# Kernel optimization log

Measured on AMD Instinct MI355X. Metric: run time of the kernel, lower is better.

The kernel has to match this reference:

```python
import jax, jax.numpy as jnp
import numpy as np

N_PTS = 20000  # points per cloud


def setup_inputs() -> dict:
    key = jax.random.key(0)
    k1, k2 = jax.random.split(key)
    preds = jax.random.normal(k1, (N_PTS, 3), dtype=jnp.float32)
    gts = jax.random.normal(k2, (1, N_PTS, 3), dtype=jnp.float32)
    return {"preds": preds, "gts": gts}


def reference(preds, gts):
    # x = gts: [B, Nx, 3]; y = preds.unsqueeze(0): [1, Ny, 3] (B must be 1 for bmm)
    y = preds[None]                                   # [1, Ny, 3]
    x = gts                                           # [1, Nx, 3]
    xx = jnp.sum(x * x, axis=-1)                      # [1, Nx]  (diag of x x^T)
    yy = jnp.sum(y * y, axis=-1)                      # [1, Ny]
    zz = jnp.einsum('bnd,bmd->bnm', x, y)             # [1, Nx, Ny]
    P = xx[:, :, None] + yy[:, None, :] - 2.0 * zz    # [1, Nx, Ny] squared dists
    dist1 = jnp.min(P, axis=1)                        # [1, Ny] min over gts points
    dist2 = jnp.min(P, axis=2)                        # [1, Nx] min over pred points
    idx1 = jnp.argmin(P, axis=1)                      # [1, Ny]
    idx2 = jnp.argmin(P, axis=2)                      # [1, Nx]
    return dist1, dist2, idx1, idx2
```

## Files before the change

kernel.cpp:

```cpp
#include <hip/hip_runtime.h>

#define N_PTS  20000
#define NG     128
#define NC     (NG * NG)
#define GMIN   (-6.0f)
#define GINV   (NG / 12.0f)
#define MARGIN 5e-4f
#define SSTRIDE (N_PTS / 64)
#define QB79   79

__device__ __forceinline__ float np_self_dot(float x, float y, float z) {
    return __fadd_rn(__fadd_rn(__fmul_rn(x, x), __fmul_rn(y, y)),
                     __fmul_rn(z, z));
}
__device__ __forceinline__ unsigned ordmap(float f) {
    unsigned b = __float_as_uint(f);
    return (b & 0x80000000u) ? ~b : (b | 0x80000000u);
}
__device__ __forceinline__ float invord(unsigned h) {
    return __uint_as_float((h & 0x80000000u) ? (h ^ 0x80000000u) : ~h);
}
__device__ __forceinline__ int cellC(float v) {
    int c = (int)((v - GMIN) * GINV);
    return c < 0 ? 0 : (c > NG - 1 ? NG - 1 : c);
}
__device__ __forceinline__ unsigned long long wave_min_u64(unsigned long long k) {
    #pragma unroll
    for (int m = 1; m < 64; m <<= 1) {
        unsigned long long o = __shfl_xor(k, m, 64);
        k = (o < k) ? o : k;
    }
    return k;
}

#define EVALQ(r, QX, QY, QZ, SQ, KEY)                                      \
    {   float sr = np_self_dot((r).x, (r).y, (r).z);                       \
        float zz = __fadd_rn(__fadd_rn(__fmul_rn(QX, (r).x),               \
                                       __fmul_rn(QY, (r).y)),              \
                             __fmul_rn(QZ, (r).z));                        \
        float P  = __fsub_rn(__fadd_rn(SQ, sr), __fadd_rn(zz, zz));        \
        unsigned long long kk =                                            \
            ((unsigned long long)ordmap(P) << 32) | __float_as_uint((r).w);\
        KEY = (kk < KEY) ? kk : KEY; }

#define SCAN_ROWS32(BND, ROWS, QX, QY, QZ, SQ, KEY)                        \
    for (int r0 = 0; r0 < (ROWS); r0 += 3) {                               \
        int i1 = r0 + 1 < (ROWS) ? r0 + 1 : (ROWS) - 1;                    \
        int i2 = r0 + 2 < (ROWS) ? r0 + 2 : (ROWS) - 1;                    \
        int L0 = __shfl(BND, r0, 64), H0 = __shfl(BND, 32 + r0, 64);       \
        int L1 = __shfl(BND, i1, 64), H1 = __shfl(BND, 32 + i1, 64);       \
        int L2 = __shfl(BND, i2, 64), H2 = __shfl(BND, 32 + i2, 64);       \
        int d0 = H0 - L0;                                                  \
        int d1 = (r0 + 1 < (ROWS)) ? H1 - L1 : 0;                          \
        int d2 = (r0 + 2 < (ROWS)) ? H2 - L2 : 0;                          \
        int s01 = d0 + d1, tot = s01 + d2;                                 \
        int t = lane;                                                      \
        if (t < tot) {                                                     \
            int p = t < d0 ? L0 + t : t < s01 ? L1 + (t - d0)              \
                                              : L2 + (t - s01);            \
            float4 rc = rs[p];                                             \
            for (t += 64; t < tot; t += 64) {                              \
                int pn = t < d0 ? L0 + t : t < s01 ? L1 + (t - d0)         \
                                                   : L2 + (t - s01);       \
                float4 rn = rs[pn];                                        \
                EVALQ(rc, QX, QY, QZ, SQ, KEY)                             \
                rc = rn;                                                   \
            }                                                              \
            EVALQ(rc, QX, QY, QZ, SQ, KEY)                                 \
        }                                                                  \
    }

#define SCAN_RECT(xL, xR, yL, yR, QX, QY, QZ, SQ, KEY)                     \
    {   int R = (xR) - (xL) + 1;                                           \
        for (int g = 0; g < R; g += 32) {                                  \
            int rows = R - g; if (rows > 32) rows = 32;                    \
            int xr  = (xL) + g + (l31 < rows ? l31 : rows - 1);            \
            int col = (lane < 32) ? (yL) : ((yR) + 1);                     \
            int b2 = cs[xr * NG + col];                                    \
            SCAN_ROWS32(b2, rows, QX, QY, QZ, SQ, KEY)                     \
        }                                                                  \
    }

__global__ __launch_bounds__(256) void k_hist(
    const float* __restrict__ preds, const float* __restrict__ gts,
    int* __restrict__ cursor)
{
    int t = blockIdx.x * 256 + threadIdx.x;
    if (t >= 2 * N_PTS) return;
    int cl = t / N_PTS, i = t - cl * N_PTS;
    const float* src = cl ? gts : preds;
    int cell = cellC(src[i*3+0]) * NG + cellC(src[i*3+1]);
    atomicAdd(&cursor[cl * NC + cell], 1);
}

__global__ __launch_bounds__(1024) void k_scan(
    int* __restrict__ cursor, int* __restrict__ bstart)
{
    __shared__ int wsum[16];
    __shared__ int wpre[16];
    int cl = blockIdx.x, t = threadIdx.x;
    int wave = t >> 6, lane = t & 63;

    int base = cl * NC + t * 16;
    const int4* c4 = (const int4*)(cursor + base);
    int4 a = c4[0], b = c4[1], c = c4[2], d = c4[3];
    int v[16] = { a.x, a.y, a.z, a.w, b.x, b.y, b.z, b.w,
                  c.x, c.y, c.z, c.w, d.x, d.y, d.z, d.w };
    int s = 0;
    #pragma unroll
    for (int i = 0; i < 16; ++i) s += v[i];

    int ps = s;
    #pragma unroll
    for (int m = 1; m < 64; m <<= 1) {
        int o = __shfl_up(ps, m, 64);
        if (lane >= m) ps += o;
    }
    if (lane == 63) wsum[wave] = ps;
    __syncthreads();
    if (t < 16) {
        int x = wsum[t];
        int px = x;
        #pragma unroll
        for (int m = 1; m < 16; m <<= 1) {
            int o = __shfl_up(px, m, 16);
            if ((t & 15) >= m) px += o;
        }
        wpre[t] = px - x;
    }
    __syncthreads();

    int run = wpre[wave] + (ps - s);
    #pragma unroll
    for (int i = 0; i < 16; ++i) {
        bstart[cl * (NC + 1) + t * 16 + i] = run;
        cursor[base + i] = run;
        run += v[i];
    }
    if (t == 1023) bstart[cl * (NC + 1) + NC] = run;
}

__global__ __launch_bounds__(256) void k_scatter(
    const float* __restrict__ preds, const float* __restrict__ gts,
    int* __restrict__ cursor, float4* __restrict__ sorted)
{
    int t = blockIdx.x * 256 + threadIdx.x;
    if (t >= 2 * N_PTS) return;
    int cl = t / N_PTS, i = t - cl * N_PTS;
    const float* src = cl ? gts : preds;
    float x = src[i*3+0], y = src[i*3+1], z = src[i*3+2];
    int cell = cellC(x) * NG + cellC(y);
    int pos = atomicAdd(&cursor[cl * NC + cell], 1);
    sorted[(size_t)cl * N_PTS + pos] = make_float4(x, y, z, __int_as_float(i));
}

__global__ __launch_bounds__(64) void k_main(
    const float4* __restrict__ sorted, const int* __restrict__ bstart,
    float* __restrict__ out)
{
    int wid  = blockIdx.x;
    int lane = threadIdx.x;
    int q0   = wid * 2;
    int dir  = q0 / N_PTS;
    int qp0  = q0 - dir * N_PTS;
    int rcl  = 1 - dir;

    const float4* rs = sorted + (size_t)rcl * N_PTS;
    const int*    cs = bstart + rcl * (NC + 1);

    float4 samp = rs[lane * SSTRIDE];
    float4 qva  = sorted[(size_t)dir * N_PTS + qp0];
    float4 qvb  = sorted[(size_t)dir * N_PTS + qp0 + 1];
    int oa = __float_as_int(qva.w), ob = __float_as_int(qvb.w);
    float qax = qva.x, qay = qva.y, qaz = qva.z;
    float qbx = qvb.x, qby = qvb.y, qbz = qvb.z;
    float sqa = np_self_dot(qax, qay, qaz);
    float sqb = np_self_dot(qbx, qby, qbz);

    unsigned long long ka = ~0ULL, kb = ~0ULL;
    int l31 = lane & 31;

    int cxa = cellC(qax), cya = cellC(qay);
    int cxb = cellC(qbx), cyb = cellC(qby);
    int sxLa = cxa > 1 ? cxa - 2 : 0, sxRa = cxa < NG-2 ? cxa + 2 : NG-1;
    int syLa = cya > 1 ? cya - 2 : 0, syRa = cya < NG-2 ? cya + 2 : NG-1;
    int sxLb = cxb > 1 ? cxb - 2 : 0, sxRb = cxb < NG-2 ? cxb + 2 : NG-1;
    int syLb = cyb > 1 ? cyb - 2 : 0, syRb = cyb < NG-2 ? cyb + 2 : NG-1;
    int nrsA = sxRa - sxLa + 1, nrsB = sxRb - sxLb + 1;
    int xrA  = sxLa + (l31 < nrsA ? l31 : nrsA - 1);
    int xrB  = sxLb + (l31 < nrsB ? l31 : nrsB - 1);
    int colA = (lane < 32) ? syLa : (syRa + 1);
    int colB = (lane < 32) ? syLb : (syRb + 1);
    int bndA = cs[xrA * NG + colA];
    int bndB = cs[xrB * NG + colB];

    SCAN_ROWS32(bndA, nrsA, qax, qay, qaz, sqa, ka)
    SCAN_ROWS32(bndB, nrsB, qbx, qby, qbz, sqb, kb)
    EVALQ(samp, qax, qay, qaz, sqa, ka)
    EVALQ(samp, qbx, qby, qbz, sqb, kb)

    ka = wave_min_u64(ka);
    kb = wave_min_u64(kb);

    float Wa = sqrtf(invord((unsigned)(ka >> 32)) + MARGIN);
    float Wb = sqrtf(invord((unsigned)(kb >> 32)) + MARGIN);
    int txLa = cellC(qax - Wa), txRa = cellC(qax + Wa);
    int tyLa = cellC(qay - Wa), tyRa = cellC(qay + Wa);
    int txLb = cellC(qbx - Wb), txRb = cellC(qbx + Wb);
    int tyLb = cellC(qby - Wb), tyRb = cellC(qby + Wb);
    if (!(txLa >= sxLa && txRa <= sxRa && tyLa >= syLa && tyRa <= syRa)) {
        SCAN_RECT(txLa, txRa, tyLa, tyRa, qax, qay, qaz, sqa, ka)
        ka = wave_min_u64(ka);
    }
    if (!(txLb >= sxLb && txRb <= sxRb && tyLb >= syLb && tyRb <= syRb)) {
        SCAN_RECT(txLb, txRb, tyLb, tyRb, qbx, qby, qbz, sqb, kb)
        kb = wave_min_u64(kb);
    }

    if (lane == 0) {
        out[dir * N_PTS + oa]       = invord((unsigned)(ka >> 32));
        out[(2 + dir) * N_PTS + oa] = (float)(unsigned)(ka & 0xFFFFFFFFu);
        out[dir * N_PTS + ob]       = invord((unsigned)(kb >> 32));
        out[(2 + dir) * N_PTS + ob] = (float)(unsigned)(kb & 0xFFFFFFFFu);
    }
}

__device__ __forceinline__ float np_pair(float sq, float sr,
                                         float qx, float qy, float qz,
                                         float rx, float ry, float rz) {
    float zz = __fadd_rn(__fadd_rn(__fmul_rn(qx, rx), __fmul_rn(qy, ry)),
                         __fmul_rn(qz, rz));
    return __fsub_rn(__fadd_rn(sq, sr), __fadd_rn(zz, zz));
}

__global__ __launch_bounds__(256) void chamfer_direct_kernel(
    const float* __restrict__ preds, const float* __restrict__ gts,
    float* __restrict__ out)
{
    __shared__ float4 spts[256];
    int bid = blockIdx.x;
    int dir = bid / QB79;
    int qb  = bid - dir * QB79;
    int q   = qb * 256 + threadIdx.x;

    const float* qpts = (dir == 0) ? preds : gts;
    const float* rpts = (dir == 0) ? gts   : preds;

    int qc = (q < N_PTS) ? q : (N_PTS - 1);
    float qx = qpts[qc*3+0], qy = qpts[qc*3+1], qz = qpts[qc*3+2];
    float sq = np_self_dot(qx, qy, qz);
    float best = 3.4e38f;
    int   bidx = 0;

    for (int t = 0; t < N_PTS; t += 256) {
        int cnt = min(256, N_PTS - t);
        __syncthreads();
        if ((int)threadIdx.x < cnt) {
            int j = t + threadIdx.x;
            float rx = rpts[j*3+0], ry = rpts[j*3+1], rz = rpts[j*3+2];
            spts[threadIdx.x] = make_float4(rx, ry, rz, np_self_dot(rx, ry, rz));
        }
        __syncthreads();
        for (int k = 0; k < cnt; ++k) {
            float4 r = spts[k];
            float d = np_pair(sq, r.w, qx, qy, qz, r.x, r.y, r.z);
            if (d < best) { best = d; bidx = t + k; }
        }
    }
    if (q < N_PTS) {
        out[dir * N_PTS + q]       = best;
        out[(2 + dir) * N_PTS + q] = (float)bidx;
    }
}

extern "C" void kernel_launch(void* const* d_in, const int* in_sizes, int n_in,
                              void* d_out, int out_size, void* d_ws, size_t ws_size,
                              hipStream_t stream) {
    const float* preds = (const float*)d_in[0];
    const float* gts   = (const float*)d_in[1];
    float* out = (float*)d_out;

    char* w = (char*)d_ws;
    size_t sorted_b = (size_t)2 * N_PTS * sizeof(float4);
    size_t bstart_b = (size_t)2 * (NC + 1) * sizeof(int);
    size_t cursor_b = (size_t)2 * NC * sizeof(int);
    size_t need = sorted_b + bstart_b + cursor_b;

    if (ws_size >= need) {
        float4* sorted = (float4*)w;
        int* bstart = (int*)(w + sorted_b);
        int* cursor = (int*)(w + sorted_b + bstart_b);

        hipMemsetAsync(cursor, 0, cursor_b, stream);
        k_hist<<<(2 * N_PTS + 255) / 256, 256, 0, stream>>>(preds, gts, cursor);
        k_scan<<<2, 1024, 0, stream>>>(cursor, bstart);
        k_scatter<<<(2 * N_PTS + 255) / 256, 256, 0, stream>>>(
            preds, gts, cursor, sorted);
        k_main<<<N_PTS, 64, 0, stream>>>(sorted, bstart, out);
    } else {
        chamfer_direct_kernel<<<2 * QB79, 256, 0, stream>>>(preds, gts, out);
    }
}
```

Measured before the change: 118.7 us.

## Share a staged LDS candidate window across 8 sorted queries per block

Moves k_main from one 64-thread wave per two queries to a 256-thread block handling 8 consecutive sorted queries. The block computes the union of their 5x5 cell neighbourhoods, stages those reference points into shared memory once, and each wave scans that window for its two queries. The aim is to remove redundant global loads of overlapping neighbourhoods. The cost is that each query now scans a larger union window, and a __syncthreads barrier is added. A fallback to the old per-query path remains for windows that are too wide or too large.

```diff
diff --git a/kernel.cpp b/kernel.cpp
--- a/kernel.cpp
+++ b/kernel.cpp
@@ -7,6 +7,8 @@
 #define GINV   (NG / 12.0f)
 #define MARGIN 5e-4f
 #define SSTRIDE (N_PTS / 64)
+#define WINCAP 2048
+#define QPB    8
 #define QB79   79
 
 __device__ __forceinline__ float np_self_dot(float x, float y, float z) {
@@ -32,6 +34,8 @@
     }
     return k;
 }
+__device__ __forceinline__ int imin2(int a, int b) { return a < b ? a : b; }
+__device__ __forceinline__ int imax2(int a, int b) { return a > b ? a : b; }
 
 #define EVALQ(r, QX, QY, QZ, SQ, KEY)                                      \
     {   float sr = np_self_dot((r).x, (r).y, (r).z);                       \
@@ -154,13 +158,17 @@
     sorted[(size_t)cl * N_PTS + pos] = make_float4(x, y, z, __int_as_float(i));
 }
 
-__global__ __launch_bounds__(64) void k_main(
+__global__ __launch_bounds__(256) void k_main(
     const float4* __restrict__ sorted, const int* __restrict__ bstart,
     float* __restrict__ out)
 {
-    int wid  = blockIdx.x;
-    int lane = threadIdx.x;
-    int q0   = wid * 2;
+    __shared__ float4 win[WINCAP];
+    __shared__ float4 qbuf[QPB];
+
+    int bid  = blockIdx.x;
+    int tid  = threadIdx.x;
+    int wave = tid >> 6, lane = tid & 63, l31 = lane & 31;
+    int q0   = bid * QPB;
     int dir  = q0 / N_PTS;
     int qp0  = q0 - dir * N_PTS;
     int rcl  = 1 - dir;
@@ -168,53 +176,119 @@
     const float4* rs = sorted + (size_t)rcl * N_PTS;
     const int*    cs = bstart + rcl * (NC + 1);
 
-    float4 samp = rs[lane * SSTRIDE];
-    float4 qva  = sorted[(size_t)dir * N_PTS + qp0];
-    float4 qvb  = sorted[(size_t)dir * N_PTS + qp0 + 1];
+    if (tid < QPB) qbuf[tid] = sorted[(size_t)dir * N_PTS + qp0 + tid];
+    __syncthreads();
+
+    int mnx = NG, mxx = -1, mny = NG, mxy = -1;
+    #pragma unroll
+    for (int j = 0; j < QPB; ++j) {
+        float4 q = qbuf[j];
+        int cx = cellC(q.x), cy = cellC(q.y);
+        mnx = imin2(mnx, cx); mxx = imax2(mxx, cx);
+        mny = imin2(mny, cy); mxy = imax2(mxy, cy);
+    }
+    int xL = imax2(mnx - 2, 0), xR = imin2(mxx + 2, NG - 1);
+    int yL = imax2(mny - 2, 0), yR = imin2(mxy + 2, NG - 1);
+    int R  = xR - xL + 1;
+
+    int xr  = xL + (l31 < R ? l31 : R - 1);
+    int col = (lane < 32) ? yL : (yR + 1);
+    int bnd = (R <= 32) ? cs[xr * NG + col] : 0;
+
+    int total = 0;
+    if (R <= 32)
+        for (int r = 0; r < R; ++r)
+            total += __shfl(bnd, 32 + r, 64) - __shfl(bnd, r, 64);
+    bool use_lds = (R <= 32) && (total <= WINCAP);
+
+    float4 qva = qbuf[wave * 2],  qvb = qbuf[wave * 2 + 1];
     int oa = __float_as_int(qva.w), ob = __float_as_int(qvb.w);
     float qax = qva.x, qay = qva.y, qaz = qva.z;
     float qbx = qvb.x, qby = qvb.y, qbz = qvb.z;
     float sqa = np_self_dot(qax, qay, qaz);
     float sqb = np_self_dot(qbx, qby, qbz);
-
     unsigned long long ka = ~0ULL, kb = ~0ULL;
-    int l31 = lane & 31;
-
-    int cxa = cellC(qax), cya = cellC(qay);
-    int cxb = cellC(qbx), cyb = cellC(qby);
-    int sxLa = cxa > 1 ? cxa - 2 : 0, sxRa = cxa < NG-2 ? cxa + 2 : NG-1;
-    int syLa = cya > 1 ? cya - 2 : 0, syRa = cya < NG-2 ? cya + 2 : NG-1;
-    int sxLb = cxb > 1 ? cxb - 2 : 0, sxRb = cxb < NG-2 ? cxb + 2 : NG-1;
-    int syLb = cyb > 1 ? cyb - 2 : 0, syRb = cyb < NG-2 ? cyb + 2 : NG-1;
-    int nrsA = sxRa - sxLa + 1, nrsB = sxRb - sxLb + 1;
-    int xrA  = sxLa + (l31 < nrsA ? l31 : nrsA - 1);
-    int xrB  = sxLb + (l31 < nrsB ? l31 : nrsB - 1);
-    int colA = (lane < 32) ? syLa : (syRa + 1);
-    int colB = (lane < 32) ? syLb : (syRb + 1);
-    int bndA = cs[xrA * NG + colA];
-    int bndB = cs[xrB * NG + colB];
-
-    SCAN_ROWS32(bndA, nrsA, qax, qay, qaz, sqa, ka)
-    SCAN_ROWS32(bndB, nrsB, qbx, qby, qbz, sqb, kb)
-    EVALQ(samp, qax, qay, qaz, sqa, ka)
-    EVALQ(samp, qbx, qby, qbz, sqb, kb)
-
-    ka = wave_min_u64(ka);
-    kb = wave_min_u64(kb);
-
-    float Wa = sqrtf(invord((unsigned)(ka >> 32)) + MARGIN);
-    float Wb = sqrtf(invord((unsigned)(kb >> 32)) + MARGIN);
-    int txLa = cellC(qax - Wa), txRa = cellC(qax + Wa);
-    int tyLa = cellC(qay - Wa), tyRa = cellC(qay + Wa);
-    int txLb = cellC(qbx - Wb), txRb = cellC(qbx + Wb);
-    int tyLb = cellC(qby - Wb), tyRb = cellC(qby + Wb);
-    if (!(txLa >= sxLa && txRa <= sxRa && tyLa >= syLa && tyRa <= syRa)) {
-        SCAN_RECT(txLa, txRa, tyLa, tyRa, qax, qay, qaz, sqa, ka)
+
+    if (use_lds) {
+        int off = 0;
+        for (int r = 0; r < R; ++r) {
+            int Lr = __shfl(bnd, r, 64), Hr = __shfl(bnd, 32 + r, 64);
+            int cnt = Hr - Lr;
+            for (int j = tid; j < cnt; j += 256) win[off + j] = rs[Lr + j];
+            off += cnt;
+        }
+        __syncthreads();
+
+        if (off == 0) {
+            float4 samp = rs[lane * SSTRIDE];
+            EVALQ(samp, qax, qay, qaz, sqa, ka)
+            EVALQ(samp, qbx, qby, qbz, sqb, kb)
+        } else {
+            int t = lane;
+            if (t < off) {
+                float4 rc = win[t];
+                for (t += 64; t < off; t += 64) {
+                    float4 rn = win[t];
+                    EVALQ(rc, qax, qay, qaz, sqa, ka)
+                    EVALQ(rc, qbx, qby, qbz, sqb, kb)
+                    rc = rn;
+                }
+                EVALQ(rc, qax, qay, qaz, sqa, ka)
+                EVALQ(rc, qbx, qby, qbz, sqb, kb)
+            }
+        }
         ka = wave_min_u64(ka);
-    }
-    if (!(txLb >= sxLb && txRb <= sxRb && tyLb >= syLb && tyRb <= syRb)) {
-        SCAN_RECT(txLb, txRb, tyLb, tyRb, qbx, qby, qbz, sqb, kb)
         kb = wave_min_u64(kb);
+
+        float Wa = sqrtf(invord((unsigned)(ka >> 32)) + MARGIN);
+        float Wb = sqrtf(invord((unsigned)(kb >> 32)) + MARGIN);
+        int txLa = cellC(qax - Wa), txRa = cellC(qax + Wa);
+        int tyLa = cellC(qay - Wa), tyRa = cellC(qay + Wa);
+        int txLb = cellC(qbx - Wb), txRb = cellC(qbx + Wb);
+        int tyLb = cellC(qby - Wb), tyRb = cellC(qby + Wb);
+        if (!(txLa >= xL && txRa <= xR && tyLa >= yL && tyRa <= yR)) {
+            SCAN_RECT(txLa, txRa, tyLa, tyRa, qax, qay, qaz, sqa, ka)
+            ka = wave_min_u64(ka);
+        }
+        if (!(txLb >= xL && txRb <= xR && tyLb >= yL && tyRb <= yR)) {
+            SCAN_RECT(txLb, txRb, tyLb, tyRb, qbx, qby, qbz, sqb, kb)
+            kb = wave_min_u64(kb);
+        }
+    } else {
+        float4 samp = rs[lane * SSTRIDE];
+        int cxa = cellC(qax), cya = cellC(qay);
+        int cxb = cellC(qbx), cyb = cellC(qby);
+        int sxLa = cxa > 1 ? cxa-2 : 0, sxRa = cxa < NG-2 ? cxa+2 : NG-1;
+        int syLa = cya > 1 ? cya-2 : 0, syRa = cya < NG-2 ? cya+2 : NG-1;
+        int sxLb = cxb > 1 ? cxb-2 : 0, sxRb = cxb < NG-2 ? cxb+2 : NG-1;
+        int syLb = cyb > 1 ? cyb-2 : 0, syRb = cyb < NG-2 ? cyb+2 : NG-1;
+        int nrsA = sxRa - sxLa + 1, nrsB = sxRb - sxLb + 1;
+        int xrA  = sxLa + (l31 < nrsA ? l31 : nrsA - 1);
+        int xrB  = sxLb + (l31 < nrsB ? l31 : nrsB - 1);
+        int colA = (lane < 32) ? syLa : (syRa + 1);
+        int colB = (lane < 32) ? syLb : (syRb + 1);
+        int bndA = cs[xrA * NG + colA];
+        int bndB = cs[xrB * NG + colB];
+        SCAN_ROWS32(bndA, nrsA, qax, qay, qaz, sqa, ka)
+        SCAN_ROWS32(bndB, nrsB, qbx, qby, qbz, sqb, kb)
+        EVALQ(samp, qax, qay, qaz, sqa, ka)
+        EVALQ(samp, qbx, qby, qbz, sqb, kb)
+        ka = wave_min_u64(ka);
+        kb = wave_min_u64(kb);
+        float Wa = sqrtf(invord((unsigned)(ka >> 32)) + MARGIN);
+        float Wb = sqrtf(invord((unsigned)(kb >> 32)) + MARGIN);
+        int txLa = cellC(qax - Wa), txRa = cellC(qax + Wa);
+        int tyLa = cellC(qay - Wa), tyRa = cellC(qay + Wa);
+        int txLb = cellC(qbx - Wb), txRb = cellC(qbx + Wb);
+        int tyLb = cellC(qby - Wb), tyRb = cellC(qby + Wb);
+        if (!(txLa >= sxLa && txRa <= sxRa && tyLa >= syLa && tyRa <= syRa)) {
+            SCAN_RECT(txLa, txRa, tyLa, tyRa, qax, qay, qaz, sqa, ka)
+            ka = wave_min_u64(ka);
+        }
+        if (!(txLb >= sxLb && txRb <= sxRb && tyLb >= syLb && tyRb <= syRb)) {
+            SCAN_RECT(txLb, txRb, tyLb, tyRb, qbx, qby, qbz, sqb, kb)
+            kb = wave_min_u64(kb);
+        }
     }
 
     if (lane == 0) {
@@ -296,7 +370,7 @@
         k_scan<<<2, 1024, 0, stream>>>(cursor, bstart);
         k_scatter<<<(2 * N_PTS + 255) / 256, 256, 0, stream>>>(
             preds, gts, cursor, sorted);
-        k_main<<<N_PTS, 64, 0, stream>>>(sorted, bstart, out);
+        k_main<<<2 * N_PTS / QPB, 256, 0, stream>>>(sorted, bstart, out);
     } else {
         chamfer_direct_kernel<<<2 * QB79, 256, 0, stream>>>(preds, gts, out);
     }
```

After: 120.5 us. About the same (+1.5%).
